# Kernel tuning notes

Measured on AMD Instinct MI355X. Metric: run time of the kernel, lower is better.

The kernel has to match this reference:

```python
import jax, jax.numpy as jnp
import numpy as np

N_NODES = 100000
N_EDGES = 3200000
IN_F, HID, NC = 384, 64, 2


def setup_inputs() -> dict:
    key = jax.random.key(0)
    ks = jax.random.split(key, 8)
    X = jax.random.normal(ks[0], (N_NODES, IN_F), dtype=jnp.float32)
    edge_index = jax.random.randint(ks[1], (2, N_EDGES), 0, N_NODES, dtype=jnp.int64)
    edge_weight = jax.random.uniform(ks[2], (N_EDGES,), dtype=jnp.float32)
    W1 = jax.random.normal(ks[3], (IN_F, HID), dtype=jnp.float32) / np.sqrt(IN_F)
    b1 = jnp.zeros((HID,), dtype=jnp.float32)
    W2 = jax.random.normal(ks[4], (HID, HID), dtype=jnp.float32) / np.sqrt(HID)
    b2 = jnp.zeros((HID,), dtype=jnp.float32)
    Wm1 = jax.random.normal(ks[5], (HID, HID), dtype=jnp.float32) / np.sqrt(HID)
    bm1 = jnp.zeros((HID,), dtype=jnp.float32)
    Wm2 = jax.random.normal(ks[6], (HID, NC), dtype=jnp.float32) / np.sqrt(HID)
    bm2 = jnp.zeros((NC,), dtype=jnp.float32)
    return {"X": X, "edge_index": edge_index, "edge_weight": edge_weight,
            "W1": W1, "b1": b1, "W2": W2, "b2": b2,
            "Wm1": Wm1, "bm1": bm1, "Wm2": Wm2, "bm2": bm2}


def _gcn_norm(edge_index, edge_weight, n):
    # add self-loops with weight 1 (PyG gcn_norm, add_self_loops=True)
    loop = jnp.arange(n, dtype=edge_index.dtype)
    row = jnp.concatenate([edge_index[0], loop])
    col = jnp.concatenate([edge_index[1], loop])
    w = jnp.concatenate([edge_weight, jnp.ones((n,), edge_weight.dtype)])
    deg = jax.ops.segment_sum(w, col, num_segments=n)
    dis = jnp.where(deg > 0, jax.lax.rsqrt(jnp.where(deg > 0, deg, 1.0)), 0.0)
    norm = dis[row] * w * dis[col]  # [E+N]
    return row, col, norm


def _gcn_conv(x, row, col, norm, W, b, n):
    h = x @ W                                   # [N, out]
    msg = norm[:, None] * h[row]                # gather + scale  [E+N, out]
    return jax.ops.segment_sum(msg, col, num_segments=n) + b


def reference(X, edge_index, edge_weight, W1, b1, W2, b2, Wm1, bm1, Wm2, bm2):
    n = X.shape[0]
    row, col, norm = _gcn_norm(edge_index, edge_weight, n)
    # PyG BasicGNN: act (leaky_relu) after all but last conv; dropout off in eval
    h = _gcn_conv(X, row, col, norm, W1, b1, n)
    h = jax.nn.leaky_relu(h, negative_slope=0.01)
    h = _gcn_conv(h, row, col, norm, W2, b2, n)
    # MLP: Linear -> Dropout(eval: identity) -> ELU -> Linear
    h = jax.nn.elu(h @ Wm1 + bm1)
    logits = h @ Wm2 + bm2
    return jax.nn.softmax(logits, axis=-1)
```

## Files before the change

### kernel.cpp

```cpp
#include <hip/hip_runtime.h>
#include <math.h>

#define NN 100000
#define NE 3200000
#define INF 384
#define HID 64
#define CAP 48
#define OVF_CAP 65536
#define NBIN 391
#define NREP 8
#define NCTR (NBIN * NREP)
#define BCAP 1536
#define EPB 8192
#define NBLK ((NE + EPB - 1) / EPB)

typedef unsigned long long ulong64;
typedef unsigned int uint32;
typedef unsigned short ushort16;
typedef __attribute__((ext_vector_type(8))) short bf16x8;
typedef __attribute__((ext_vector_type(4))) float f32x4;

__device__ inline float bf16_to_f(uint32 us) { return __uint_as_float(us << 16); }
__device__ inline ushort16 f_to_bf16(float f) {
    uint32 u = __float_as_uint(f);
    u += 0x7FFF + ((u >> 16) & 1);
    return (ushort16)(u >> 16);
}
__device__ inline void split_bf16(float x, ushort16& h, ushort16& l) {
    h = f_to_bf16(x);
    float hf = bf16_to_f((uint32)h);
    l = f_to_bf16(x - hf);
}


__global__ __launch_bounds__(256) void setup_kernel(const float* __restrict__ W1,
                                                    const float* __restrict__ W2,
                                                    const float* __restrict__ Wm1,
                                                    ushort16* __restrict__ wp1h,
                                                    ushort16* __restrict__ wp1l,
                                                    ushort16* __restrict__ wp2h,
                                                    ushort16* __restrict__ wp2l,
                                                    ushort16* __restrict__ wpm1h,
                                                    ushort16* __restrict__ wpm1l,
                                                    int* __restrict__ ovf_cnt,
                                                    int* __restrict__ bincur) {
    int i = blockIdx.x * blockDim.x + threadIdx.x;
    int np = gridDim.x * blockDim.x;
    if (i == 0) *ovf_cnt = 0;
    for (int idx = i; idx < NCTR; idx += np) bincur[idx] = idx * BCAP;
    for (int idx = i; idx < INF * HID; idx += np) {
        int k = idx >> 6, j = idx & 63;
        ushort16 h, l;
        split_bf16(W1[idx], h, l);
        size_t dst = ((size_t)(((k >> 5) * 4 + (j >> 4)) * 64 +
                               ((j & 15) | (((k >> 3) & 3) << 4))) << 3) + (k & 7);
        wp1h[dst] = h;
        wp1l[dst] = l;
    }
    for (int idx = i; idx < HID * HID; idx += np) {
        int k = idx >> 6, j = idx & 63;
        size_t dst = ((size_t)(((k >> 5) * 4 + (j >> 4)) * 64 +
                               ((j & 15) | (((k >> 3) & 3) << 4))) << 3) + (k & 7);
        ushort16 h, l;
        split_bf16(W2[idx], h, l);
        wp2h[dst] = h;
        wp2l[dst] = l;
        split_bf16(Wm1[idx], h, l);
        wpm1h[dst] = h;
        wpm1l[dst] = l;
    }
}


__global__ __launch_bounds__(1024) void binscatter_kernel(const int* __restrict__ row,
                                                          const int* __restrict__ col,
                                                          const float* __restrict__ ew,
                                                          int* __restrict__ bincur,
                                                          ulong64* __restrict__ ebin) {
    __shared__ int lhist[NBIN];
    __shared__ int lbase[NBIN];
    int tid = threadIdx.x;
    int rep = blockIdx.x & (NREP - 1);
    int base = blockIdx.x * EPB;
    if (tid < NBIN) lhist[tid] = 0;
    __syncthreads();
    int brk[8], rr[8];
    uint32 wb[8];
#pragma unroll
    for (int i = 0; i < 8; i++) {
        int e = base + i * 1024 + tid;
        brk[i] = -1;
        if (e < NE) {
            int r = row[e];
            int c = col[e];
            wb[i] = __float_as_uint(ew[e]);
            int b = c >> 8;
            int rk = atomicAdd(&lhist[b], 1);
            brk[i] = (b << 16) | rk;
            rr[i] = r | ((c & 255) << 17);
        }
    }
    __syncthreads();
    if (tid < NBIN && lhist[tid] > 0)
        lbase[tid] = atomicAdd(&bincur[tid * NREP + rep], lhist[tid]);
    __syncthreads();
#pragma unroll
    for (int i = 0; i < 8; i++) {
        if (brk[i] >= 0) {
            int b = brk[i] >> 16;
            int pos = lbase[b] + (brk[i] & 0xFFFF);
            int lim = (b * NREP + rep + 1) * BCAP;
            if (pos < lim)
                ebin[pos] = ((ulong64)wb[i] << 32) | (uint32)rr[i];
        }
    }
}


__global__ __launch_bounds__(256) void bucket_kernel(const int* __restrict__ bincur,
                                                     const ulong64* __restrict__ ebin,
                                                     ulong64* __restrict__ sedge,
                                                     int* __restrict__ cnt,
                                                     float* __restrict__ dis,
                                                     int* __restrict__ ovf_cnt,
                                                     int4* __restrict__ ovf) {
    __shared__ int cur[256];
    __shared__ float sdeg[256];
    int bin = blockIdx.x;
    int node0 = bin << 8;
    cur[threadIdx.x] = 0;
    sdeg[threadIdx.x] = 0.f;
    __syncthreads();
    for (int rep = 0; rep < NREP; rep++) {
        int ctr = bin * NREP + rep;
        int start = ctr * BCAP;
        int end = min(bincur[ctr], start + BCAP);
        for (int i = start + threadIdx.x; i < end; i += 256) {
            ulong64 pk = ebin[i];
            int r = (int)(pk & 0x1FFFF);
            int lc = (int)((pk >> 17) & 255);
            uint32 wb = (uint32)(pk >> 32);
            atomicAdd(&sdeg[lc], __uint_as_float(wb));
            int rank = atomicAdd(&cur[lc], 1);
            int node = node0 + lc;
            if (rank < CAP) {
                sedge[(size_t)node * CAP + rank] = ((ulong64)wb << 32) | (uint32)r;
            } else {
                int o = atomicAdd(ovf_cnt, 1);
                if (o < OVF_CAP) ovf[o] = make_int4(r, node, (int)wb, 0);
            }
        }
    }
    __syncthreads();
    int node = node0 + threadIdx.x;
    if (node < NN) {
        int cc = min(cur[threadIdx.x], CAP);
        cnt[node] = cc;
        int cpad = min((cc + 7) & ~7, CAP);
        for (int s = cc; s < cpad; s++) sedge[(size_t)node * CAP + s] = 0;
        dis[node] = rsqrtf(sdeg[threadIdx.x] + 1.0f);
    }
}


template <int K, bool LEAKY>
__global__ __launch_bounds__(256, 3) void mfma_gemm_kernel(const float* __restrict__ A,
                                                           const ushort16* __restrict__ Wph,
                                                           const ushort16* __restrict__ Wpl,
                                                           const float* __restrict__ dis,
                                                           ushort16* __restrict__ out) {
    const int tid = threadIdx.x;
    const int w = tid >> 6;
    const int l = tid & 63;
    const int lrow = l & 15;
    const int kq = (l >> 4) * 8;
    const int nb = blockIdx.x * 128;
    const int wr = nb + w * 32;
    const bf16x8* __restrict__ Bh = (const bf16x8*)Wph;
    const bf16x8* __restrict__ Bl = (const bf16x8*)Wpl;
    const float* __restrict__ ar0 = A + (size_t)min(wr + lrow, NN - 1) * K + kq;
    const float* __restrict__ ar1 = A + (size_t)min(wr + 16 + lrow, NN - 1) * K + kq;

    f32x4 acc[2][4];
#pragma unroll
    for (int m = 0; m < 2; m++)
#pragma unroll
        for (int n = 0; n < 4; n++) acc[m][n] = (f32x4){0.f, 0.f, 0.f, 0.f};

    constexpr int NS = K / 32;
    float4 a0[2], a1[2];
    a0[0] = *(const float4*)(ar0);
    a1[0] = *(const float4*)(ar0 + 4);
    a0[1] = *(const float4*)(ar1);
    a1[1] = *(const float4*)(ar1 + 4);

#pragma unroll
    for (int ks = 0; ks < NS; ks++) {
        bf16x8 bhc[4], blc[4];
#pragma unroll
        for (int n = 0; n < 4; n++) {
            bhc[n] = Bh[(size_t)(ks * 4 + n) * 64 + l];
            blc[n] = Bl[(size_t)(ks * 4 + n) * 64 + l];
        }
        float4 p0[2], p1[2];
        if (ks + 1 < NS) {
            p0[0] = *(const float4*)(ar0 + (ks + 1) * 32);
            p1[0] = *(const float4*)(ar0 + (ks + 1) * 32 + 4);
            p0[1] = *(const float4*)(ar1 + (ks + 1) * 32);
            p1[1] = *(const float4*)(ar1 + (ks + 1) * 32 + 4);
        }
        bf16x8 ah[2], al[2];
#pragma unroll
        for (int m = 0; m < 2; m++) {
            float av[8] = {a0[m].x, a0[m].y, a0[m].z, a0[m].w,
                           a1[m].x, a1[m].y, a1[m].z, a1[m].w};
#pragma unroll
            for (int i = 0; i < 8; i++) {
                float x = av[i];
                if (LEAKY) x = x > 0.f ? x : 0.01f * x;
                ushort16 hh, ll;
                split_bf16(x, hh, ll);
                ah[m][i] = (short)hh;
                al[m][i] = (short)ll;
            }
        }
#pragma unroll
        for (int n = 0; n < 4; n++)
#pragma unroll
            for (int m = 0; m < 2; m++) {
                acc[m][n] = __builtin_amdgcn_mfma_f32_16x16x32_bf16(ah[m], bhc[n], acc[m][n], 0, 0, 0);
                acc[m][n] = __builtin_amdgcn_mfma_f32_16x16x32_bf16(al[m], bhc[n], acc[m][n], 0, 0, 0);
                acc[m][n] = __builtin_amdgcn_mfma_f32_16x16x32_bf16(ah[m], blc[n], acc[m][n], 0, 0, 0);
            }
        if (ks + 1 < NS) {
#pragma unroll
            for (int m = 0; m < 2; m++) {
                a0[m] = p0[m];
                a1[m] = p1[m];
            }
        }
    }
#pragma unroll
    for (int m = 0; m < 2; m++) {
        int rbase = wr + m * 16 + (l >> 4) * 4;
#pragma unroll
        for (int r = 0; r < 4; r++) {
            int node = rbase + r;
            if (node < NN) {
                float ds = dis[node];
#pragma unroll
                for (int n = 0; n < 4; n++)
                    out[(size_t)node * HID + n * 16 + lrow] = f_to_bf16(acc[m][n][r] * ds);
            }
        }
    }
}


__global__ __launch_bounds__(256) void aggregate_kernel(const int* __restrict__ cnt,
                                                        const ulong64* __restrict__ sedge,
                                                        const float* __restrict__ dis,
                                                        const ushort16* __restrict__ hs,
                                                        const float* __restrict__ bias,
                                                        float* __restrict__ out) {
    int lane = threadIdx.x & 63;
    int wslot = __builtin_amdgcn_readfirstlane(threadIdx.x >> 6);
    int n = blockIdx.x * 4 + wslot;
    if (n >= NN) return;
    int c = cnt[n];
    int cpad = (c + 7) & ~7;
    float dn = dis[n];
    const ulong64* __restrict__ el = sedge + (size_t)n * CAP;

    float acc = bf16_to_f((uint32)hs[(size_t)n * HID + lane]);
    if (cpad > 0) {
        ulong64 p[8];
#pragma unroll
        for (int i = 0; i < 8; i++) p[i] = el[i];
        int j = 0;
        for (;;) {
            int jn = j + 8;
            bool more = jn < cpad;
            ulong64 q[8];
            if (more) {
#pragma unroll
                for (int i = 0; i < 8; i++) q[i] = el[jn + i];
            }
            float v[8], wv[8];
#pragma unroll
            for (int i = 0; i < 8; i++) {
                uint32 r = (uint32)p[i];
                wv[i] = __uint_as_float((uint32)(p[i] >> 32));
                v[i] = bf16_to_f((uint32)hs[(size_t)r * HID + lane]);
            }
#pragma unroll
            for (int i = 0; i < 8; i++) acc = fmaf(wv[i], v[i], acc);
            if (!more) break;
            j = jn;
#pragma unroll
            for (int i = 0; i < 8; i++) p[i] = q[i];
        }
    }
    out[(size_t)n * HID + lane] = fmaf(dn, acc, bias[lane]);
}


__global__ __launch_bounds__(256) void ovf_kernel(const int* __restrict__ ovf_cnt,
                                                  const int4* __restrict__ ovf,
                                                  const float* __restrict__ dis,
                                                  const ushort16* __restrict__ hs,
                                                  float* __restrict__ out) {
    int lane = threadIdx.x & 63;
    int wid = blockIdx.x * 4 + (threadIdx.x >> 6);
    int nw = gridDim.x * 4;
    int c = min(*ovf_cnt, OVF_CAP);
    for (int i = wid; i < c; i += nw) {
        int4 t = ovf[i];
        float w = __int_as_float(t.z);
        float nrm = w * dis[t.y];
        atomicAdd(&out[(size_t)t.y * HID + lane],
                  nrm * bf16_to_f((uint32)hs[(size_t)t.x * HID + lane]));
    }
}


__global__ __launch_bounds__(256, 3) void mlp_mfma_kernel(const float* __restrict__ agg,
                                                          const ushort16* __restrict__ Wph,
                                                          const ushort16* __restrict__ Wpl,
                                                          const float* __restrict__ bm1,
                                                          const float* __restrict__ Wm2,
                                                          const float* __restrict__ bm2,
                                                          float* __restrict__ out) {
    const int tid = threadIdx.x;
    const int w = tid >> 6;
    const int l = tid & 63;
    const int lrow = l & 15;
    const int kq = (l >> 4) * 8;
    const int nb = blockIdx.x * 128;
    const int wr = nb + w * 32;
    const bf16x8* __restrict__ Bh = (const bf16x8*)Wph;
    const bf16x8* __restrict__ Bl = (const bf16x8*)Wpl;
    const float* __restrict__ ar0 = agg + (size_t)min(wr + lrow, NN - 1) * HID + kq;
    const float* __restrict__ ar1 = agg + (size_t)min(wr + 16 + lrow, NN - 1) * HID + kq;

    bf16x8 bh[8], bl[8];
#pragma unroll
    for (int s = 0; s < 8; s++) {
        bh[s] = Bh[(size_t)s * 64 + l];
        bl[s] = Bl[(size_t)s * 64 + l];
    }
    float4 a[2][4];
#pragma unroll
    for (int m = 0; m < 2; m++) {
        const float* ar = m ? ar1 : ar0;
        a[m][0] = *(const float4*)(ar);
        a[m][1] = *(const float4*)(ar + 4);
        a[m][2] = *(const float4*)(ar + 32);
        a[m][3] = *(const float4*)(ar + 36);
    }

    f32x4 acc[2][4];
#pragma unroll
    for (int m = 0; m < 2; m++)
#pragma unroll
        for (int n = 0; n < 4; n++) acc[m][n] = (f32x4){0.f, 0.f, 0.f, 0.f};

#pragma unroll
    for (int ks = 0; ks < 2; ks++) {
        bf16x8 ah[2], al[2];
#pragma unroll
        for (int m = 0; m < 2; m++) {
            float4 x0 = a[m][ks * 2], x1 = a[m][ks * 2 + 1];
            float av[8] = {x0.x, x0.y, x0.z, x0.w, x1.x, x1.y, x1.z, x1.w};
#pragma unroll
            for (int i = 0; i < 8; i++) {
                ushort16 hh, ll;
                split_bf16(av[i], hh, ll);
                ah[m][i] = (short)hh;
                al[m][i] = (short)ll;
            }
        }
#pragma unroll
        for (int n = 0; n < 4; n++)
#pragma unroll
            for (int m = 0; m < 2; m++) {
                acc[m][n] = __builtin_amdgcn_mfma_f32_16x16x32_bf16(ah[m], bh[ks * 4 + n], acc[m][n], 0, 0, 0);
                acc[m][n] = __builtin_amdgcn_mfma_f32_16x16x32_bf16(al[m], bh[ks * 4 + n], acc[m][n], 0, 0, 0);
                acc[m][n] = __builtin_amdgcn_mfma_f32_16x16x32_bf16(ah[m], bl[ks * 4 + n], acc[m][n], 0, 0, 0);
            }
    }

    float b1c[4], w2a[4], w2b[4];
#pragma unroll
    for (int n = 0; n < 4; n++) {
        int colw = n * 16 + lrow;
        b1c[n] = bm1[colw];
        w2a[n] = Wm2[colw * 2];
        w2b[n] = Wm2[colw * 2 + 1];
    }
    float b20 = bm2[0], b21 = bm2[1];

#pragma unroll
    for (int m = 0; m < 2; m++)
#pragma unroll
        for (int r = 0; r < 4; r++) {
            float s0 = 0.f, s1 = 0.f;
#pragma unroll
            for (int n = 0; n < 4; n++) {
                float u = acc[m][n][r] + b1c[n];
                u = u > 0.f ? u : (expf(u) - 1.f);
                s0 = fmaf(u, w2a[n], s0);
                s1 = fmaf(u, w2b[n], s1);
            }
#pragma unroll
            for (int off = 1; off < 16; off <<= 1) {
                s0 += __shfl_xor(s0, off);
                s1 += __shfl_xor(s1, off);
            }
            int node = wr + m * 16 + (l >> 4) * 4 + r;
            if (lrow == 0 && node < NN) {
                float l0 = s0 + b20, l1 = s1 + b21;
                float mx = fmaxf(l0, l1);
                float e0 = expf(l0 - mx), e1 = expf(l1 - mx);
                float inv = 1.f / (e0 + e1);
                *(float2*)&out[(size_t)node * 2] = make_float2(e0 * inv, e1 * inv);
            }
        }
}


extern "C" void kernel_launch(void* const* d_in, const int* in_sizes, int n_in,
                              void* d_out, int out_size, void* d_ws, size_t ws_size,
                              hipStream_t stream) {
    const float* X   = (const float*)d_in[0];
    const int*   ei  = (const int*)d_in[1];
    const float* ew  = (const float*)d_in[2];
    const float* W1  = (const float*)d_in[3];
    const float* b1  = (const float*)d_in[4];
    const float* W2  = (const float*)d_in[5];
    const float* b2  = (const float*)d_in[6];
    const float* Wm1 = (const float*)d_in[7];
    const float* bm1 = (const float*)d_in[8];
    const float* Wm2 = (const float*)d_in[9];
    const float* bm2 = (const float*)d_in[10];
    const int* row = ei;
    const int* col = ei + NE;
    float* out = (float*)d_out;

    const size_t MB = 1024 * 1024;
    const size_t KB = 1024;
    char* ws = (char*)d_ws;
    float*    dis     = (float*)   (ws + 0 * MB);
    int*      cnt     = (int*)     (ws + 1 * MB);
    ushort16* wp1h    = (ushort16*)(ws + 2 * MB);
    ushort16* wp1l    = (ushort16*)(ws + 2 * MB + 64 * KB);
    ushort16* wp2h    = (ushort16*)(ws + 2 * MB + 128 * KB);
    ushort16* wp2l    = (ushort16*)(ws + 2 * MB + 144 * KB);
    ushort16* wpm1h   = (ushort16*)(ws + 2 * MB + 160 * KB);
    ushort16* wpm1l   = (ushort16*)(ws + 2 * MB + 176 * KB);
    int*      ovf_cnt = (int*)     (ws + 3 * MB);
    int*      bincur  = (int*)     (ws + 3 * MB + 16 * KB);
    int4*     ovf     = (int4*)    (ws + 4 * MB);
    ulong64*  ebin    = (ulong64*) (ws + 5 * MB);
    float*    h2      = (float*)   (ws + 5 * MB);
    ulong64*  sedge   = (ulong64*) (ws + 44 * MB);
    ushort16* h1      = (ushort16*)(ws + 83 * MB);

    setup_kernel<<<64, 256, 0, stream>>>(W1, W2, Wm1, wp1h, wp1l, wp2h, wp2l,
                                         wpm1h, wpm1l, ovf_cnt, bincur);
    binscatter_kernel<<<NBLK, 1024, 0, stream>>>(row, col, ew, bincur, ebin);
    bucket_kernel<<<NBIN, 256, 0, stream>>>(bincur, ebin, sedge, cnt, dis, ovf_cnt, ovf);

    mfma_gemm_kernel<INF, false><<<(NN + 127) / 128, 256, 0, stream>>>(X, wp1h, wp1l, dis, h1);
    aggregate_kernel<<<(NN + 3) / 4, 256, 0, stream>>>(cnt, sedge, dis, h1, b1, h2);
    ovf_kernel<<<256, 256, 0, stream>>>(ovf_cnt, ovf, dis, h1, h2);

    mfma_gemm_kernel<HID, true><<<(NN + 127) / 128, 256, 0, stream>>>(h2, wp2h, wp2l, dis, h1);
    aggregate_kernel<<<(NN + 3) / 4, 256, 0, stream>>>(cnt, sedge, dis, h1, b2, h2);
    ovf_kernel<<<256, 256, 0, stream>>>(ovf_cnt, ovf, dis, h1, h2);

    mlp_mfma_kernel<<<(NN + 127) / 128, 256, 0, stream>>>(h2, wpm1h, wpm1l, bm1, Wm2, bm2, out);
}
```

Baseline: 506.9 us.

## Stage GEMM A tiles into LDS via direct global-to-LDS loads with double buffering

The X@W GEMM now streams 64x64 fp32 tiles of A into shared memory with global_load_lds, double-buffered and XOR-swizzled to avoid bank conflicts. Each wave handles 16 rows instead of 32, so blocks cover 64 nodes and twice as many blocks launch. The aim is fully coalesced row loads and better overlap of memory with MFMA work than the old per-lane strided register loads. In exchange it uses 32KB of LDS per block, adds barriers each tile, and drops the 3-waves-per-SIMD occupancy hint.

```diff
diff --git a/kernel.cpp b/kernel.cpp
--- a/kernel.cpp
+++ b/kernel.cpp
@@ -30,6 +30,12 @@
     h = f_to_bf16(x);
     float hf = bf16_to_f((uint32)h);
     l = f_to_bf16(x - hf);
+}
+
+__device__ inline void gload_lds16(const float* g, float* l) {
+    __builtin_amdgcn_global_load_lds(
+        (const __attribute__((address_space(1))) void*)g,
+        (__attribute__((address_space(3))) void*)l, 16, 0, 0);
 }
 
 
@@ -164,94 +170,98 @@
 
 
 template <int K, bool LEAKY>
-__global__ __launch_bounds__(256, 3) void mfma_gemm_kernel(const float* __restrict__ A,
-                                                           const ushort16* __restrict__ Wph,
-                                                           const ushort16* __restrict__ Wpl,
-                                                           const float* __restrict__ dis,
-                                                           ushort16* __restrict__ out) {
+__global__ __launch_bounds__(256) void mfma_gemm_kernel(const float* __restrict__ A,
+                                                        const ushort16* __restrict__ Wph,
+                                                        const ushort16* __restrict__ Wpl,
+                                                        const float* __restrict__ dis,
+                                                        ushort16* __restrict__ out) {
+    __shared__ float xs[2][64 * 64];
     const int tid = threadIdx.x;
     const int w = tid >> 6;
     const int l = tid & 63;
     const int lrow = l & 15;
-    const int kq = (l >> 4) * 8;
-    const int nb = blockIdx.x * 128;
-    const int wr = nb + w * 32;
+    const int c4 = l >> 4;
+    const int nb = blockIdx.x * 64;
     const bf16x8* __restrict__ Bh = (const bf16x8*)Wph;
     const bf16x8* __restrict__ Bl = (const bf16x8*)Wpl;
-    const float* __restrict__ ar0 = A + (size_t)min(wr + lrow, NN - 1) * K + kq;
-    const float* __restrict__ ar1 = A + (size_t)min(wr + 16 + lrow, NN - 1) * K + kq;
-
-    f32x4 acc[2][4];
-#pragma unroll
-    for (int m = 0; m < 2; m++)
-#pragma unroll
-        for (int n = 0; n < 4; n++) acc[m][n] = (f32x4){0.f, 0.f, 0.f, 0.f};
-
-    constexpr int NS = K / 32;
-    float4 a0[2], a1[2];
-    a0[0] = *(const float4*)(ar0);
-    a1[0] = *(const float4*)(ar0 + 4);
-    a0[1] = *(const float4*)(ar1);
-    a1[1] = *(const float4*)(ar1 + 4);
-
-#pragma unroll
-    for (int ks = 0; ks < NS; ks++) {
-        bf16x8 bhc[4], blc[4];
-#pragma unroll
-        for (int n = 0; n < 4; n++) {
-            bhc[n] = Bh[(size_t)(ks * 4 + n) * 64 + l];
-            blc[n] = Bl[(size_t)(ks * 4 + n) * 64 + l];
-        }
-        float4 p0[2], p1[2];
-        if (ks + 1 < NS) {
-            p0[0] = *(const float4*)(ar0 + (ks + 1) * 32);
-            p1[0] = *(const float4*)(ar0 + (ks + 1) * 32 + 4);
-            p0[1] = *(const float4*)(ar1 + (ks + 1) * 32);
-            p1[1] = *(const float4*)(ar1 + (ks + 1) * 32 + 4);
-        }
-        bf16x8 ah[2], al[2];
-#pragma unroll
-        for (int m = 0; m < 2; m++) {
-            float av[8] = {a0[m].x, a0[m].y, a0[m].z, a0[m].w,
-                           a1[m].x, a1[m].y, a1[m].z, a1[m].w};
+
+    int srow[4], soff[4];
+#pragma unroll
+    for (int c = 0; c < 4; c++) {
+        int r = w * 16 + c * 4 + (l >> 4);
+        srow[c] = r;
+        soff[c] = ((l & 15) ^ (r & 7)) * 4;
+    }
+
+    f32x4 acc[4];
+#pragma unroll
+    for (int n = 0; n < 4; n++) acc[n] = (f32x4){0.f, 0.f, 0.f, 0.f};
+
+    constexpr int NT = K / 64;
+    const int R = w * 16 + lrow;
+    const int sw = R & 7;
+    const float* __restrict__ lrowp = &xs[0][0] + (size_t)R * 64;
+
+#pragma unroll
+    for (int c = 0; c < 4; c++) {
+        int gr = min(nb + srow[c], NN - 1);
+        gload_lds16(A + (size_t)gr * K + soff[c], &xs[0][(w * 16 + c * 4) * 64]);
+    }
+    __syncthreads();
+
+    int cur = 0;
+    for (int t = 0; t < NT; t++) {
+        if (t + 1 < NT) {
+#pragma unroll
+            for (int c = 0; c < 4; c++) {
+                int gr = min(nb + srow[c], NN - 1);
+                gload_lds16(A + (size_t)gr * K + (t + 1) * 64 + soff[c],
+                            &xs[cur ^ 1][(w * 16 + c * 4) * 64]);
+            }
+        }
+        const float* __restrict__ rp = lrowp + (size_t)cur * 64 * 64;
+#pragma unroll
+        for (int ks = 0; ks < 2; ks++) {
+            int kslot = t * 2 + ks;
+            bf16x8 bhc[4], blc[4];
+#pragma unroll
+            for (int n = 0; n < 4; n++) {
+                bhc[n] = Bh[(size_t)(kslot * 4 + n) * 64 + l];
+                blc[n] = Bl[(size_t)(kslot * 4 + n) * 64 + l];
+            }
+            int m0 = ks * 8 + c4 * 2;
+            float4 f0 = *(const float4*)(rp + ((m0 ^ sw) << 2));
+            float4 f1 = *(const float4*)(rp + (((m0 + 1) ^ sw) << 2));
+            float av[8] = {f0.x, f0.y, f0.z, f0.w, f1.x, f1.y, f1.z, f1.w};
+            bf16x8 ah, al;
 #pragma unroll
             for (int i = 0; i < 8; i++) {
                 float x = av[i];
                 if (LEAKY) x = x > 0.f ? x : 0.01f * x;
                 ushort16 hh, ll;
                 split_bf16(x, hh, ll);
-                ah[m][i] = (short)hh;
-                al[m][i] = (short)ll;
-            }
-        }
-#pragma unroll
-        for (int n = 0; n < 4; n++)
-#pragma unroll
-            for (int m = 0; m < 2; m++) {
-                acc[m][n] = __builtin_amdgcn_mfma_f32_16x16x32_bf16(ah[m], bhc[n], acc[m][n], 0, 0, 0);
-                acc[m][n] = __builtin_amdgcn_mfma_f32_16x16x32_bf16(al[m], bhc[n], acc[m][n], 0, 0, 0);
-                acc[m][n] = __builtin_amdgcn_mfma_f32_16x16x32_bf16(ah[m], blc[n], acc[m][n], 0, 0, 0);
-            }
-        if (ks + 1 < NS) {
-#pragma unroll
-            for (int m = 0; m < 2; m++) {
-                a0[m] = p0[m];
-                a1[m] = p1[m];
-            }
-        }
-    }
-#pragma unroll
-    for (int m = 0; m < 2; m++) {
-        int rbase = wr + m * 16 + (l >> 4) * 4;
-#pragma unroll
-        for (int r = 0; r < 4; r++) {
-            int node = rbase + r;
-            if (node < NN) {
-                float ds = dis[node];
-#pragma unroll
-                for (int n = 0; n < 4; n++)
-                    out[(size_t)node * HID + n * 16 + lrow] = f_to_bf16(acc[m][n][r] * ds);
-            }
+                ah[i] = (short)hh;
+                al[i] = (short)ll;
+            }
+#pragma unroll
+            for (int n = 0; n < 4; n++) {
+                acc[n] = __builtin_amdgcn_mfma_f32_16x16x32_bf16(ah, bhc[n], acc[n], 0, 0, 0);
+                acc[n] = __builtin_amdgcn_mfma_f32_16x16x32_bf16(al, bhc[n], acc[n], 0, 0, 0);
+                acc[n] = __builtin_amdgcn_mfma_f32_16x16x32_bf16(ah, blc[n], acc[n], 0, 0, 0);
+            }
+        }
+        __syncthreads();
+        cur ^= 1;
+    }
+    int rbase = nb + w * 16 + (l >> 4) * 4;
+#pragma unroll
+    for (int r = 0; r < 4; r++) {
+        int node = rbase + r;
+        if (node < NN) {
+            float ds = dis[node];
+#pragma unroll
+            for (int n = 0; n < 4; n++)
+                out[(size_t)node * HID + n * 16 + lrow] = f_to_bf16(acc[n][r] * ds);
         }
     }
 }
@@ -471,11 +481,11 @@
     binscatter_kernel<<<NBLK, 1024, 0, stream>>>(row, col, ew, bincur, ebin);
     bucket_kernel<<<NBIN, 256, 0, stream>>>(bincur, ebin, sedge, cnt, dis, ovf_cnt, ovf);
 
-    mfma_gemm_kernel<INF, false><<<(NN + 127) / 128, 256, 0, stream>>>(X, wp1h, wp1l, dis, h1);
+    mfma_gemm_kernel<INF, false><<<(NN + 63) / 64, 256, 0, stream>>>(X, wp1h, wp1l, dis, h1);
     aggregate_kernel<<<(NN + 3) / 4, 256, 0, stream>>>(cnt, sedge, dis, h1, b1, h2);
     ovf_kernel<<<256, 256, 0, stream>>>(ovf_cnt, ovf, dis, h1, h2);
 
-    mfma_gemm_kernel<HID, true><<<(NN + 127) / 128, 256, 0, stream>>>(h2, wp2h, wp2l, dis, h1);
+    mfma_gemm_kernel<HID, true><<<(NN + 63) / 64, 256, 0, stream>>>(h2, wp2h, wp2l, dis, h1);
     aggregate_kernel<<<(NN + 3) / 4, 256, 0, stream>>>(cnt, sedge, dis, h1, b2, h2);
     ovf_kernel<<<256, 256, 0, stream>>>(ovf_cnt, ovf, dis, h1, h2);
 
```

Measured after the change: 490.3 us. 3.3% less time.
